# Optimization experiments

Hardware: AMD Instinct MI355X
Metric: run time of the kernel (lower is better)

Reference implementation:

```python
import jax, jax.numpy as jnp
import numpy as np

B, T, D, H = 8, 2048, 1024, 1024

def setup_inputs() -> dict:
    key = jax.random.key(0)
    k1, k2, k3, k4 = jax.random.split(key, 4)
    scale = 1.0 / np.sqrt(D)
    return {
        "x": jax.random.normal(k1, (B, T, D), dtype=jnp.float32),
        "Wq": jax.random.normal(k2, (D, H), dtype=jnp.float32) * scale,
        "Wk": jax.random.normal(k3, (D, H), dtype=jnp.float32) * scale,
        "Wv": jax.random.normal(k4, (D, H), dtype=jnp.float32) * scale,
    }

def reference(x, Wq, Wk, Wv):
    # Single-head causal self-attention (dropout in eval mode = identity)
    q = jnp.einsum('btd,dh->bth', x, Wq)
    k = jnp.einsum('btd,dh->bth', x, Wk)
    v = jnp.einsum('btd,dh->bth', x, Wv)
    inv_sqrt_h = 1.0 / jnp.sqrt(jnp.asarray(q.shape[-1], q.dtype))
    scores = jnp.einsum('bqh,bkh->bqk', q, k) * inv_sqrt_h  # [B, T, T]
    Tq = scores.shape[-1]
    causal = jnp.tril(jnp.ones((Tq, Tq), dtype=bool))
    scores = jnp.where(causal, scores, jnp.asarray(-jnp.inf, scores.dtype))
    weights = jax.nn.softmax(scores, axis=-1)
    return jnp.einsum('bqk,bkh->bqh', weights, v)
```

## Files before the change

kernel.cpp:

```cpp
#include <hip/hip_runtime.h>

#define Bn 8
#define Tn 2048
#define Dn 1024
#define Hn 1024
#define Mn (Bn * Tn)

typedef __attribute__((ext_vector_type(8))) short bf16x8;
typedef __attribute__((ext_vector_type(4))) short short4v;
typedef __attribute__((ext_vector_type(16))) float f32x16;

__device__ __forceinline__ unsigned short f2bf(float f) {
  union { float f; unsigned int u; } v; v.f = f;
  unsigned int u = v.u;
  u += 0x7FFFu + ((u >> 16) & 1u);
  return (unsigned short)(u >> 16);
}
__device__ __forceinline__ float bf2f(unsigned short h) {
  union { unsigned int u; float f; } v; v.u = ((unsigned int)h) << 16;
  return v.f;
}

__device__ __forceinline__ void gload_lds16(const unsigned short* g, unsigned short* l) {
  __builtin_amdgcn_global_load_lds((const __attribute__((address_space(1))) void*)g,
                                   (__attribute__((address_space(3))) void*)l, 16, 0, 0);
}

__device__ __forceinline__ void stage128x32s(const unsigned short* gbase, size_t row_stride,
                                             unsigned short* lds, int wave, int lane) {
#pragma unroll
  for (int c = 0; c < 2; ++c) {
    int rl = c * 16 + (lane >> 2);
    int pos = (lane & 3) ^ (rl & 3);
    const unsigned short* g = gbase + (size_t)(wave * 32 + rl) * row_stride + pos * 8;
    gload_lds16(g, lds + (wave * 32 + c * 16) * 32);
  }
}
__device__ __forceinline__ void stage128x64s(const unsigned short* gbase, size_t row_stride,
                                             unsigned short* lds0, unsigned short* lds1,
                                             int wave, int lane) {
  stage128x32s(gbase, row_stride, lds0, wave, lane);
  stage128x32s(gbase + 32, row_stride, lds1, wave, lane);
}

__device__ __forceinline__ void mma_bk32(const unsigned short* lA, const unsigned short* lB,
                                         int wr, int wc, int l32, int half,
                                         f32x16 acc[2][2]) {
#pragma unroll
  for (int kk = 0; kk < 2; ++kk) {
    const int pos = (kk * 2 + half) ^ (l32 & 3);
    bf16x8 af[2], bfr[2];
#pragma unroll
    for (int m = 0; m < 2; ++m)
      af[m] = *(const bf16x8*)&lA[(wr + m * 32 + l32) * 32 + pos * 8];
#pragma unroll
    for (int n = 0; n < 2; ++n)
      bfr[n] = *(const bf16x8*)&lB[(wc + n * 32 + l32) * 32 + pos * 8];
#pragma unroll
    for (int m = 0; m < 2; ++m)
#pragma unroll
      for (int n = 0; n < 2; ++n)
        acc[m][n] = __builtin_amdgcn_mfma_f32_32x32x16_bf16(af[m], bfr[n], acc[m][n], 0, 0, 0);
  }
}

__global__ __launch_bounds__(256) void k_convert(const float* __restrict__ in,
                                                 unsigned short* __restrict__ out, int n4) {
  int idx = blockIdx.x * 256 + threadIdx.x;
  if (idx >= n4) return;
  float4 v = ((const float4*)in)[idx];
  short4v o;
  o.x = (short)f2bf(v.x); o.y = (short)f2bf(v.y);
  o.z = (short)f2bf(v.z); o.w = (short)f2bf(v.w);
  *(short4v*)(out + (size_t)idx * 4) = o;
}

__global__ __launch_bounds__(256) void k_cvt_w_t(const float* __restrict__ W0,
                                                 const float* __restrict__ W1,
                                                 const float* __restrict__ W2,
                                                 unsigned short* __restrict__ Wt3) {
  const int n0 = blockIdx.x * 64, k0 = blockIdx.y * 64, w = blockIdx.z;
  const float* W = (w == 0) ? W0 : (w == 1) ? W1 : W2;
  unsigned short* Wt = Wt3 + (size_t)w * Hn * Dn;
  __shared__ unsigned short lT[64 * 65];
  const int tid = threadIdx.x;
#pragma unroll
  for (int p = 0; p < 2; ++p) {
    int o = tid + p * 256;
    int r = o >> 3, c = (o & 7) * 8;
    const float* src = W + (size_t)(k0 + r) * Hn + n0 + c;
    float4 v0 = *(const float4*)src;
    float4 v1 = *(const float4*)(src + 4);
    unsigned short* d = &lT[r * 65 + c];
    d[0] = f2bf(v0.x); d[1] = f2bf(v0.y); d[2] = f2bf(v0.z); d[3] = f2bf(v0.w);
    d[4] = f2bf(v1.x); d[5] = f2bf(v1.y); d[6] = f2bf(v1.z); d[7] = f2bf(v1.w);
  }
  __syncthreads();
#pragma unroll
  for (int p = 0; p < 2; ++p) {
    int o = tid + p * 256;
    int r2 = o >> 3, c2 = (o & 7) * 8;
    bf16x8 v;
#pragma unroll
    for (int s = 0; s < 8; ++s) v[s] = (short)lT[(c2 + s) * 65 + r2];
    *(bf16x8*)(Wt + (size_t)(n0 + r2) * Dn + k0 + c2) = v;
  }
}

__global__ __launch_bounds__(256) void gemm_qkv(const unsigned short* __restrict__ A,
                                                const unsigned short* __restrict__ Wt3,
                                                unsigned short* __restrict__ Q,
                                                unsigned short* __restrict__ Kb,
                                                unsigned short* __restrict__ Vt) {
  const int f = blockIdx.x;
  const int c = f & 7;
  const int q = f >> 3;
  const int nn = q % 24;
  const int w = nn >> 3;
  const int n0 = (nn & 7) * 128;
  const int m0 = ((q / 24) * 8 + c) * 128;
  const unsigned short* B = Wt3 + (size_t)w * Hn * Dn;
  __shared__ unsigned short lA[2][128 * 32];
  __shared__ unsigned short lB[2][128 * 32];
  const int tid = threadIdx.x;
  const int lane = tid & 63, wave = tid >> 6;
  const int wr = (wave >> 1) * 64, wc = (wave & 1) * 64;
  const int l32 = lane & 31, half = lane >> 5;

  f32x16 acc[2][2];
#pragma unroll
  for (int m = 0; m < 2; ++m)
#pragma unroll
    for (int n = 0; n < 2; ++n) acc[m][n] = (f32x16)(0.f);

  for (int kt = 0; kt < Dn / 64; ++kt) {
    stage128x64s(A + (size_t)m0 * Dn + kt * 64, Dn, lA[0], lA[1], wave, lane);
    stage128x64s(B + (size_t)n0 * Dn + kt * 64, Dn, lB[0], lB[1], wave, lane);
    __syncthreads();
    mma_bk32(lA[0], lB[0], wr, wc, l32, half, acc);
    mma_bk32(lA[1], lB[1], wr, wc, l32, half, acc);
    __syncthreads();
  }
  if (w != 2) {
    unsigned short* C = (w == 0) ? Q : Kb;
#pragma unroll
    for (int m = 0; m < 2; ++m)
#pragma unroll
      for (int n = 0; n < 2; ++n) {
        int col = n0 + wc + n * 32 + l32;
#pragma unroll
        for (int qd = 0; qd < 4; ++qd) {
          int rb = m0 + wr + m * 32 + 8 * qd + 4 * half;
#pragma unroll
          for (int rr = 0; rr < 4; ++rr)
            C[(size_t)(rb + rr) * Hn + col] = f2bf(acc[m][n][qd * 4 + rr]);
        }
      }
  } else {
    const int bb = m0 >> 11;
    const int tb = m0 & 2047;
#pragma unroll
    for (int m = 0; m < 2; ++m)
#pragma unroll
      for (int n = 0; n < 2; ++n) {
        int h = n0 + wc + n * 32 + l32;
#pragma unroll
        for (int qd = 0; qd < 4; ++qd) {
          int t0 = tb + wr + m * 32 + 8 * qd + 4 * half;
          short4v o;
          o.x = (short)f2bf(acc[m][n][qd * 4 + 0]);
          o.y = (short)f2bf(acc[m][n][qd * 4 + 1]);
          o.z = (short)f2bf(acc[m][n][qd * 4 + 2]);
          o.w = (short)f2bf(acc[m][n][qd * 4 + 3]);
          *(short4v*)(Vt + ((size_t)bb * Hn + h) * Tn + t0) = o;
        }
      }
  }
}

__global__ __launch_bounds__(256) void gemm_scores(const unsigned short* __restrict__ Q,
                                                   const unsigned short* __restrict__ K,
                                                   unsigned short* __restrict__ S) {
  const int f = blockIdx.x;
  const int b = f & 7;
  const int q = f >> 3;
  const int rt = 15 - (q & 15);
  const int ct = q >> 4;
  if (ct > rt) return;
  const int j0 = ct * 128, i0 = rt * 128;
  const unsigned short* Qb = Q + (size_t)b * Tn * Hn;
  const unsigned short* Kp = K + (size_t)b * Tn * Hn;
  unsigned short* Sb = S + (size_t)b * Tn * Tn;
  __shared__ unsigned short lA[2][128 * 32];
  __shared__ unsigned short lB[2][128 * 32];
  const int tid = threadIdx.x;
  const int lane = tid & 63, wave = tid >> 6;
  const int wr = (wave >> 1) * 64, wc = (wave & 1) * 64;
  const int l32 = lane & 31, half = lane >> 5;

  f32x16 acc[2][2];
#pragma unroll
  for (int m = 0; m < 2; ++m)
#pragma unroll
    for (int n = 0; n < 2; ++n) acc[m][n] = (f32x16)(0.f);

  for (int kt = 0; kt < Hn / 64; ++kt) {
    stage128x64s(Qb + (size_t)i0 * Hn + kt * 64, Hn, lA[0], lA[1], wave, lane);
    stage128x64s(Kp + (size_t)j0 * Hn + kt * 64, Hn, lB[0], lB[1], wave, lane);
    __syncthreads();
    mma_bk32(lA[0], lB[0], wr, wc, l32, half, acc);
    mma_bk32(lA[1], lB[1], wr, wc, l32, half, acc);
    __syncthreads();
  }
#pragma unroll
  for (int m = 0; m < 2; ++m)
#pragma unroll
    for (int n = 0; n < 2; ++n) {
      int col = j0 + wc + n * 32 + l32;
#pragma unroll
      for (int qd = 0; qd < 4; ++qd) {
        int rb = i0 + wr + m * 32 + 8 * qd + 4 * half;
#pragma unroll
        for (int rr = 0; rr < 4; ++rr) {
          int row = rb + rr;
          float e = (col <= row) ? __expf(acc[m][n][qd * 4 + rr] * 0.03125f) : 0.f;
          Sb[(size_t)row * Tn + col] = f2bf(e);
        }
      }
    }
}

__global__ __launch_bounds__(256) void k_rowsum(const unsigned short* __restrict__ S,
                                                float* __restrict__ l) {
  const int b = blockIdx.y;
  const int i = blockIdx.x * 4 + (threadIdx.x >> 6);
  const int lane = threadIdx.x & 63;
  const unsigned short* row = S + ((size_t)b * Tn + i) * (size_t)Tn;
  const int npad = ((i >> 7) + 1) << 7;
  float s = 0.f;
  for (int j0 = 0; j0 < npad; j0 += 512) {
    int j = j0 + lane * 8;
    if (j < npad) {
      bf16x8 v = *(const bf16x8*)(row + j);
#pragma unroll
      for (int t = 0; t < 8; ++t) s += bf2f((unsigned short)v[t]);
    }
  }
#pragma unroll
  for (int off = 32; off > 0; off >>= 1) s += __shfl_down(s, off);
  if (lane == 0) l[(size_t)b * Tn + i] = s;
}

__global__ __launch_bounds__(256) void gemm_out(const unsigned short* __restrict__ P,
                                                const unsigned short* __restrict__ Vt,
                                                const float* __restrict__ lbuf,
                                                float* __restrict__ O) {
  const int f = blockIdx.x;
  const int b = f & 7;
  const int q = f >> 3;
  const int n0 = (q & 7) * 128;
  const int rt = 15 - (q >> 3);
  const int i0 = rt * 128;
  const int nkt = (rt + 1) * 2;
  const unsigned short* Pb = P + (size_t)b * Tn * Tn;
  const unsigned short* Vb = Vt + (size_t)b * Tn * Hn;
  __shared__ unsigned short lA[2][128 * 32];
  __shared__ unsigned short lB[2][128 * 32];
  const int tid = threadIdx.x;
  const int lane = tid & 63, wave = tid >> 6;
  const int wr = (wave >> 1) * 64, wc = (wave & 1) * 64;
  const int l32 = lane & 31, half = lane >> 5;

  f32x16 acc[2][2];
#pragma unroll
  for (int m = 0; m < 2; ++m)
#pragma unroll
    for (int n = 0; n < 2; ++n) acc[m][n] = (f32x16)(0.f);

  for (int kt = 0; kt < nkt; ++kt) {
    stage128x64s(Pb + (size_t)i0 * Tn + kt * 64, Tn, lA[0], lA[1], wave, lane);
    stage128x64s(Vb + (size_t)n0 * Tn + kt * 64, Tn, lB[0], lB[1], wave, lane);
    __syncthreads();
    mma_bk32(lA[0], lB[0], wr, wc, l32, half, acc);
    mma_bk32(lA[1], lB[1], wr, wc, l32, half, acc);
    __syncthreads();
  }
#pragma unroll
  for (int m = 0; m < 2; ++m)
#pragma unroll
    for (int n = 0; n < 2; ++n) {
      int col = n0 + wc + n * 32 + l32;
#pragma unroll
      for (int qd = 0; qd < 4; ++qd) {
        int rb = i0 + wr + m * 32 + 8 * qd + 4 * half;
        float4 lv = *(const float4*)&lbuf[(size_t)b * Tn + rb];
#pragma unroll
        for (int rr = 0; rr < 4; ++rr) {
          float inv = 1.f / ((&lv.x)[rr]);
          O[((size_t)b * Tn + rb + rr) * Hn + col] = acc[m][n][qd * 4 + rr] * inv;
        }
      }
    }
}

extern "C" void kernel_launch(void* const* d_in, const int* in_sizes, int n_in,
                              void* d_out, int out_size, void* d_ws, size_t ws_size,
                              hipStream_t stream) {
  const float* x  = (const float*)d_in[0];
  const float* Wq = (const float*)d_in[1];
  const float* Wk = (const float*)d_in[2];
  const float* Wv = (const float*)d_in[3];
  float* out = (float*)d_out;

  char* ws = (char*)d_ws;
  const size_t MiB = 1024 * 1024;
  unsigned short* Wt3 = (unsigned short*)(ws + 0 * MiB);
  unsigned short* xb  = (unsigned short*)(ws + 6 * MiB);
  unsigned short* Qb  = (unsigned short*)(ws + 38 * MiB);
  unsigned short* Kb  = (unsigned short*)(ws + 70 * MiB);
  unsigned short* Vt  = (unsigned short*)(ws + 102 * MiB);
  unsigned short* S   = (unsigned short*)(ws + 134 * MiB);
  float*          lrow = (float*)(ws + 6 * MiB);

  {
    int n4 = (Mn * Dn) / 4;
    k_convert<<<dim3(n4 / 256), 256, 0, stream>>>(x, xb, n4);
  }
  {
    dim3 g(Hn / 64, Dn / 64, 3);
    k_cvt_w_t<<<g, 256, 0, stream>>>(Wq, Wk, Wv, Wt3);
  }
  {
    gemm_qkv<<<dim3(3072), 256, 0, stream>>>(xb, Wt3, Qb, Kb, Vt);
  }
  {
    gemm_scores<<<dim3(2048), 256, 0, stream>>>(Qb, Kb, S);
  }
  {
    k_rowsum<<<dim3(Tn / 4, Bn), 256, 0, stream>>>(S, lrow);
  }
  {
    gemm_out<<<dim3(1024), 256, 0, stream>>>(S, Vt, lrow, out);
  }
}
```

Baseline: 373.3 us.

## Retile QKV GEMM to 256x256 blocks with double-buffered LDS pipeline

The QKV projection GEMM moves from 128x128 tiles with 256 threads to 256x256 tiles with 512 threads, 16x16x32 MFMAs and a 128x64 per-wave sub-tile. A double-buffered global-to-LDS pipeline overlaps the next K-slice load with compute, using explicit vmcnt waits and s_setprio around MFMA bursts. The LDS swizzle gains an extra XOR term to reduce bank conflicts; this swizzle is shared with the other GEMMs. The aim is more data reuse per tile and hidden load latency, at the cost of higher register and LDS pressure and fewer blocks.

New measurement: 349.2 us. -6.4%, faster.

```diff
diff --git a/kernel.cpp b/kernel.cpp
--- a/kernel.cpp
+++ b/kernel.cpp
@@ -9,6 +9,7 @@
 typedef __attribute__((ext_vector_type(8))) short bf16x8;
 typedef __attribute__((ext_vector_type(4))) short short4v;
 typedef __attribute__((ext_vector_type(16))) float f32x16;
+typedef __attribute__((ext_vector_type(4))) float f32x4;
 
 __device__ __forceinline__ unsigned short f2bf(float f) {
   union { float f; unsigned int u; } v; v.f = f;
@@ -26,12 +27,13 @@
                                    (__attribute__((address_space(3))) void*)l, 16, 0, 0);
 }
 
+
 __device__ __forceinline__ void stage128x32s(const unsigned short* gbase, size_t row_stride,
                                              unsigned short* lds, int wave, int lane) {
 #pragma unroll
   for (int c = 0; c < 2; ++c) {
     int rl = c * 16 + (lane >> 2);
-    int pos = (lane & 3) ^ (rl & 3);
+    int pos = (lane & 3) ^ (rl & 3) ^ ((rl >> 2) & 3);
     const unsigned short* g = gbase + (size_t)(wave * 32 + rl) * row_stride + pos * 8;
     gload_lds16(g, lds + (wave * 32 + c * 16) * 32);
   }
@@ -43,12 +45,23 @@
   stage128x32s(gbase + 32, row_stride, lds1, wave, lane);
 }
 
+__device__ __forceinline__ void stage256x32s(const unsigned short* gbase, size_t row_stride,
+                                             unsigned short* lds, int wave, int lane) {
+#pragma unroll
+  for (int c = 0; c < 2; ++c) {
+    int rl = c * 16 + (lane >> 2);
+    int pos = (lane & 3) ^ (rl & 3) ^ ((rl >> 2) & 3);
+    const unsigned short* g = gbase + (size_t)(wave * 32 + rl) * row_stride + pos * 8;
+    gload_lds16(g, lds + (wave * 32 + c * 16) * 32);
+  }
+}
+
 __device__ __forceinline__ void mma_bk32(const unsigned short* lA, const unsigned short* lB,
                                          int wr, int wc, int l32, int half,
                                          f32x16 acc[2][2]) {
 #pragma unroll
   for (int kk = 0; kk < 2; ++kk) {
-    const int pos = (kk * 2 + half) ^ (l32 & 3);
+    const int pos = (kk * 2 + half) ^ (l32 & 3) ^ ((l32 >> 2) & 3);
     bf16x8 af[2], bfr[2];
 #pragma unroll
     for (int m = 0; m < 2; ++m)
@@ -107,74 +120,149 @@
   }
 }
 
-__global__ __launch_bounds__(256) void gemm_qkv(const unsigned short* __restrict__ A,
-                                                const unsigned short* __restrict__ Wt3,
-                                                unsigned short* __restrict__ Q,
-                                                unsigned short* __restrict__ Kb,
-                                                unsigned short* __restrict__ Vt) {
+__global__ __launch_bounds__(512, 2) void gemm_qkv(const unsigned short* __restrict__ A,
+                                                   const unsigned short* __restrict__ Wt3,
+                                                   unsigned short* __restrict__ Q,
+                                                   unsigned short* __restrict__ Kb,
+                                                   unsigned short* __restrict__ Vt) {
   const int f = blockIdx.x;
   const int c = f & 7;
   const int q = f >> 3;
-  const int nn = q % 24;
-  const int w = nn >> 3;
-  const int n0 = (nn & 7) * 128;
-  const int m0 = ((q / 24) * 8 + c) * 128;
-  const unsigned short* B = Wt3 + (size_t)w * Hn * Dn;
-  __shared__ unsigned short lA[2][128 * 32];
-  __shared__ unsigned short lB[2][128 * 32];
+  const int nn = q % 12;
+  const int w = nn >> 2;
+  const int n0 = (nn & 3) * 256;
+  const int m0 = ((q / 12) * 8 + c) * 256;
+  const unsigned short* Bw = Wt3 + (size_t)w * Hn * Dn;
+  __shared__ unsigned short lds[2][4][256 * 32];
   const int tid = threadIdx.x;
   const int lane = tid & 63, wave = tid >> 6;
-  const int wr = (wave >> 1) * 64, wc = (wave & 1) * 64;
-  const int l32 = lane & 31, half = lane >> 5;
-
-  f32x16 acc[2][2];
-#pragma unroll
-  for (int m = 0; m < 2; ++m)
-#pragma unroll
-    for (int n = 0; n < 2; ++n) acc[m][n] = (f32x16)(0.f);
-
-  for (int kt = 0; kt < Dn / 64; ++kt) {
-    stage128x64s(A + (size_t)m0 * Dn + kt * 64, Dn, lA[0], lA[1], wave, lane);
-    stage128x64s(B + (size_t)n0 * Dn + kt * 64, Dn, lB[0], lB[1], wave, lane);
-    __syncthreads();
-    mma_bk32(lA[0], lB[0], wr, wc, l32, half, acc);
-    mma_bk32(lA[1], lB[1], wr, wc, l32, half, acc);
-    __syncthreads();
-  }
+  const int wr = (wave >> 2) * 128;
+  const int wc = (wave & 3) * 64;
+  const int rl15 = lane & 15, l4 = lane >> 4;
+  const int csw = (l4 ^ (lane & 3) ^ ((lane >> 2) & 3)) & 3;
+
+  f32x4 acc[8][4];
+#pragma unroll
+  for (int m = 0; m < 8; ++m)
+#pragma unroll
+    for (int n = 0; n < 4; ++n) acc[m][n] = (f32x4)(0.f);
+
+  const unsigned short* Ab = A + (size_t)m0 * Dn;
+  const unsigned short* Bb = Bw + (size_t)n0 * Dn;
+
+  auto stage_tile = [&](int kt, int d) {
+#pragma unroll
+    for (int h = 0; h < 2; ++h) {
+      stage256x32s(Ab + kt * 64 + h * 32, Dn, &lds[d][h][0], wave, lane);
+      stage256x32s(Bb + kt * 64 + h * 32, Dn, &lds[d][2 + h][0], wave, lane);
+    }
+  };
+
+  auto compute_tile = [&](int d) {
+    const unsigned short* pa = &lds[d][0][0];
+    const unsigned short* pb = &lds[d][2][0];
+    bf16x8 af[4][2], bf[4][2];
+#pragma unroll
+    for (int m = 0; m < 4; ++m)
+#pragma unroll
+      for (int h = 0; h < 2; ++h)
+        af[m][h] = *(const bf16x8*)&pa[h * 8192 + (wr + m * 16 + rl15) * 32 + csw * 8];
+#pragma unroll
+    for (int n = 0; n < 2; ++n)
+#pragma unroll
+      for (int h = 0; h < 2; ++h)
+        bf[n][h] = *(const bf16x8*)&pb[h * 8192 + (wc + n * 16 + rl15) * 32 + csw * 8];
+    __builtin_amdgcn_s_setprio(1);
+#pragma unroll
+    for (int m = 0; m < 4; ++m)
+#pragma unroll
+      for (int n = 0; n < 2; ++n)
+#pragma unroll
+        for (int h = 0; h < 2; ++h)
+          acc[m][n] = __builtin_amdgcn_mfma_f32_16x16x32_bf16(af[m][h], bf[n][h], acc[m][n], 0, 0, 0);
+    __builtin_amdgcn_s_setprio(0);
+#pragma unroll
+    for (int n = 2; n < 4; ++n)
+#pragma unroll
+      for (int h = 0; h < 2; ++h)
+        bf[n][h] = *(const bf16x8*)&pb[h * 8192 + (wc + n * 16 + rl15) * 32 + csw * 8];
+    __builtin_amdgcn_s_setprio(1);
+#pragma unroll
+    for (int m = 0; m < 4; ++m)
+#pragma unroll
+      for (int n = 2; n < 4; ++n)
+#pragma unroll
+        for (int h = 0; h < 2; ++h)
+          acc[m][n] = __builtin_amdgcn_mfma_f32_16x16x32_bf16(af[m][h], bf[n][h], acc[m][n], 0, 0, 0);
+    __builtin_amdgcn_s_setprio(0);
+#pragma unroll
+    for (int m = 0; m < 4; ++m)
+#pragma unroll
+      for (int h = 0; h < 2; ++h)
+        af[m][h] = *(const bf16x8*)&pa[h * 8192 + (wr + (m + 4) * 16 + rl15) * 32 + csw * 8];
+    __builtin_amdgcn_s_setprio(1);
+#pragma unroll
+    for (int m = 0; m < 4; ++m)
+#pragma unroll
+      for (int n = 2; n < 4; ++n)
+#pragma unroll
+        for (int h = 0; h < 2; ++h)
+          acc[m + 4][n] = __builtin_amdgcn_mfma_f32_16x16x32_bf16(af[m][h], bf[n][h], acc[m + 4][n], 0, 0, 0);
+    __builtin_amdgcn_s_setprio(0);
+    __builtin_amdgcn_s_setprio(1);
+#pragma unroll
+    for (int m = 0; m < 4; ++m)
+#pragma unroll
+      for (int n = 0; n < 2; ++n)
+#pragma unroll
+        for (int h = 0; h < 2; ++h)
+          acc[m + 4][n] = __builtin_amdgcn_mfma_f32_16x16x32_bf16(af[m][h], bf[n][h], acc[m + 4][n], 0, 0, 0);
+    __builtin_amdgcn_s_setprio(0);
+  };
+
+  stage_tile(0, 0);
+  for (int kt = 0; kt < Dn / 64 - 1; ++kt) {
+    const int d = kt & 1;
+    __builtin_amdgcn_s_barrier();
+    stage_tile(kt + 1, d ^ 1);
+    asm volatile("s_waitcnt vmcnt(8)" ::: "memory");
+    __builtin_amdgcn_s_barrier();
+    compute_tile(d);
+  }
+  asm volatile("s_waitcnt vmcnt(0)" ::: "memory");
+  __builtin_amdgcn_s_barrier();
+  compute_tile(1);
+
   if (w != 2) {
-    unsigned short* C = (w == 0) ? Q : Kb;
-#pragma unroll
-    for (int m = 0; m < 2; ++m)
-#pragma unroll
-      for (int n = 0; n < 2; ++n) {
-        int col = n0 + wc + n * 32 + l32;
-#pragma unroll
-        for (int qd = 0; qd < 4; ++qd) {
-          int rb = m0 + wr + m * 32 + 8 * qd + 4 * half;
-#pragma unroll
-          for (int rr = 0; rr < 4; ++rr)
-            C[(size_t)(rb + rr) * Hn + col] = f2bf(acc[m][n][qd * 4 + rr]);
-        }
+    unsigned short* Cp = (w == 0) ? Q : Kb;
+#pragma unroll
+    for (int m = 0; m < 8; ++m) {
+      const int row = m0 + wr + m * 16 + l4 * 4;
+#pragma unroll
+      for (int n = 0; n < 4; ++n) {
+        const int col = n0 + wc + n * 16 + rl15;
+#pragma unroll
+        for (int r = 0; r < 4; ++r)
+          Cp[(size_t)(row + r) * Hn + col] = f2bf(acc[m][n][r]);
       }
+    }
   } else {
     const int bb = m0 >> 11;
     const int tb = m0 & 2047;
 #pragma unroll
-    for (int m = 0; m < 2; ++m)
-#pragma unroll
-      for (int n = 0; n < 2; ++n) {
-        int h = n0 + wc + n * 32 + l32;
-#pragma unroll
-        for (int qd = 0; qd < 4; ++qd) {
-          int t0 = tb + wr + m * 32 + 8 * qd + 4 * half;
-          short4v o;
-          o.x = (short)f2bf(acc[m][n][qd * 4 + 0]);
-          o.y = (short)f2bf(acc[m][n][qd * 4 + 1]);
-          o.z = (short)f2bf(acc[m][n][qd * 4 + 2]);
-          o.w = (short)f2bf(acc[m][n][qd * 4 + 3]);
-          *(short4v*)(Vt + ((size_t)bb * Hn + h) * Tn + t0) = o;
-        }
+    for (int m = 0; m < 8; ++m) {
+      const int t0 = tb + wr + m * 16 + l4 * 4;
+#pragma unroll
+      for (int n = 0; n < 4; ++n) {
+        const int h = n0 + wc + n * 16 + rl15;
+        short4v o;
+        o.x = (short)f2bf(acc[m][n][0]);
+        o.y = (short)f2bf(acc[m][n][1]);
+        o.z = (short)f2bf(acc[m][n][2]);
+        o.w = (short)f2bf(acc[m][n][3]);
+        *(short4v*)(Vt + ((size_t)bb * Hn + h) * Tn + t0) = o;
       }
+    }
   }
 }
 
@@ -331,7 +419,7 @@
     k_cvt_w_t<<<g, 256, 0, stream>>>(Wq, Wk, Wv, Wt3);
   }
   {
-    gemm_qkv<<<dim3(3072), 256, 0, stream>>>(xb, Wt3, Qb, Kb, Vt);
+    gemm_qkv<<<dim3(768), 512, 0, stream>>>(xb, Wt3, Qb, Kb, Vt);
   }
   {
     gemm_scores<<<dim3(2048), 256, 0, stream>>>(Qb, Kb, S);
```

## Use single-wave 128x128 tiles with async double-buffered LDS and fused rowsum

Applied to the files above, without the earlier changes.

All three GEMMs now run on one 64-thread wave per 128x128 tile. Each wave holds an 8x8 grid of 16x16x32 MFMA accumulators and double-buffers LDS using global_load_lds, with vmcnt waits in place of __syncthreads. The scores kernel launches only the causal lower-triangle tiles, indexed with a triangular mapping, and folds the row-sum into its epilogue via atomics, which removes the separate rowsum kernel. In exchange each block has far fewer threads, uses very high register pressure from 256 accumulator floats, and gives up occupancy and latency hiding.

New measurement: 453.2 us. +21.4%, slower.

```diff
diff --git a/kernel.cpp b/kernel.cpp
--- a/kernel.cpp
+++ b/kernel.cpp
@@ -8,7 +8,7 @@
 
 typedef __attribute__((ext_vector_type(8))) short bf16x8;
 typedef __attribute__((ext_vector_type(4))) short short4v;
-typedef __attribute__((ext_vector_type(16))) float f32x16;
+typedef __attribute__((ext_vector_type(4))) float f32x4;
 
 __device__ __forceinline__ unsigned short f2bf(float f) {
   union { float f; unsigned int u; } v; v.f = f;
@@ -26,43 +26,50 @@
                                    (__attribute__((address_space(3))) void*)l, 16, 0, 0);
 }
 
-__device__ __forceinline__ void stage128x32s(const unsigned short* gbase, size_t row_stride,
-                                             unsigned short* lds, int wave, int lane) {
-#pragma unroll
-  for (int c = 0; c < 2; ++c) {
+
+__device__ __forceinline__ void stg128(const unsigned short* g, size_t stride,
+                                       unsigned short* lds, int lane) {
+#pragma unroll
+  for (int c = 0; c < 8; ++c) {
     int rl = c * 16 + (lane >> 2);
-    int pos = (lane & 3) ^ (rl & 3);
-    const unsigned short* g = gbase + (size_t)(wave * 32 + rl) * row_stride + pos * 8;
-    gload_lds16(g, lds + (wave * 32 + c * 16) * 32);
-  }
-}
-__device__ __forceinline__ void stage128x64s(const unsigned short* gbase, size_t row_stride,
-                                             unsigned short* lds0, unsigned short* lds1,
-                                             int wave, int lane) {
-  stage128x32s(gbase, row_stride, lds0, wave, lane);
-  stage128x32s(gbase + 32, row_stride, lds1, wave, lane);
-}
-
-__device__ __forceinline__ void mma_bk32(const unsigned short* lA, const unsigned short* lB,
-                                         int wr, int wc, int l32, int half,
-                                         f32x16 acc[2][2]) {
-#pragma unroll
-  for (int kk = 0; kk < 2; ++kk) {
-    const int pos = (kk * 2 + half) ^ (l32 & 3);
-    bf16x8 af[2], bfr[2];
-#pragma unroll
-    for (int m = 0; m < 2; ++m)
-      af[m] = *(const bf16x8*)&lA[(wr + m * 32 + l32) * 32 + pos * 8];
-#pragma unroll
-    for (int n = 0; n < 2; ++n)
-      bfr[n] = *(const bf16x8*)&lB[(wc + n * 32 + l32) * 32 + pos * 8];
-#pragma unroll
-    for (int m = 0; m < 2; ++m)
-#pragma unroll
-      for (int n = 0; n < 2; ++n)
-        acc[m][n] = __builtin_amdgcn_mfma_f32_32x32x16_bf16(af[m], bfr[n], acc[m][n], 0, 0, 0);
-  }
-}
+    int pos = (lane & 3) ^ (rl & 3) ^ ((rl >> 2) & 3);
+    gload_lds16(g + (size_t)rl * stride + pos * 8, lds + c * 16 * 32);
+  }
+}
+
+__device__ __forceinline__ void rd8(const unsigned short* p, int rl15, int csw, bf16x8 fr[8]) {
+#pragma unroll
+  for (int m = 0; m < 8; ++m)
+    fr[m] = *(const bf16x8*)&p[(m * 16 + rl15) * 32 + csw * 8];
+}
+
+#define W_VM16 asm volatile("s_waitcnt vmcnt(16)" ::: "memory")
+#define W_VM0  asm volatile("s_waitcnt vmcnt(0)" ::: "memory")
+#define W_LGKM0 asm volatile("s_waitcnt lgkmcnt(0)" ::: "memory")
+
+#define KLOOP(Ag, sA, Bg, sB, nt, lds, lane, rl15, csw, acc)                              \
+  {                                                                                        \
+    stg128((Ag), (sA), &(lds)[0][0][0], lane);                                             \
+    stg128((Bg), (sB), &(lds)[0][1][0], lane);                                             \
+    _Pragma("unroll 1")                                                                    \
+    for (int t = 0; t < (nt); ++t) {                                                       \
+      W_LGKM0;                                                                             \
+      const int ts = (t + 1 < (nt)) ? t + 1 : (nt)-1;                                      \
+      stg128((Ag) + (size_t)ts * 32, (sA), &(lds)[(t + 1) & 1][0][0], lane);               \
+      stg128((Bg) + (size_t)ts * 32, (sB), &(lds)[(t + 1) & 1][1][0], lane);               \
+      W_VM16;                                                                              \
+      bf16x8 a[8], b[8];                                                                   \
+      rd8(&(lds)[t & 1][0][0], rl15, csw, a);                                              \
+      rd8(&(lds)[t & 1][1][0], rl15, csw, b);                                              \
+      _Pragma("unroll")                                                                    \
+      for (int m = 0; m < 8; ++m)                                                          \
+        _Pragma("unroll")                                                                  \
+        for (int n = 0; n < 8; ++n)                                                        \
+          acc[m][n] = __builtin_amdgcn_mfma_f32_16x16x32_bf16(a[m], b[n], acc[m][n], 0, 0, 0); \
+    }                                                                                      \
+    W_VM0;                                                                                 \
+    W_LGKM0;                                                                               \
+  }
 
 __global__ __launch_bounds__(256) void k_convert(const float* __restrict__ in,
                                                  unsigned short* __restrict__ out, int n4) {
@@ -107,11 +114,11 @@
   }
 }
 
-__global__ __launch_bounds__(256) void gemm_qkv(const unsigned short* __restrict__ A,
-                                                const unsigned short* __restrict__ Wt3,
-                                                unsigned short* __restrict__ Q,
-                                                unsigned short* __restrict__ Kb,
-                                                unsigned short* __restrict__ Vt) {
+__global__ __launch_bounds__(64, 1) void gemm_qkv(const unsigned short* __restrict__ A,
+                                                  const unsigned short* __restrict__ Wt3,
+                                                  unsigned short* __restrict__ Q,
+                                                  unsigned short* __restrict__ Kb,
+                                                  unsigned short* __restrict__ Vt) {
   const int f = blockIdx.x;
   const int c = f & 7;
   const int q = f >> 3;
@@ -119,188 +126,148 @@
   const int w = nn >> 3;
   const int n0 = (nn & 7) * 128;
   const int m0 = ((q / 24) * 8 + c) * 128;
-  const unsigned short* B = Wt3 + (size_t)w * Hn * Dn;
-  __shared__ unsigned short lA[2][128 * 32];
-  __shared__ unsigned short lB[2][128 * 32];
-  const int tid = threadIdx.x;
-  const int lane = tid & 63, wave = tid >> 6;
-  const int wr = (wave >> 1) * 64, wc = (wave & 1) * 64;
-  const int l32 = lane & 31, half = lane >> 5;
-
-  f32x16 acc[2][2];
-#pragma unroll
-  for (int m = 0; m < 2; ++m)
-#pragma unroll
-    for (int n = 0; n < 2; ++n) acc[m][n] = (f32x16)(0.f);
-
-  for (int kt = 0; kt < Dn / 64; ++kt) {
-    stage128x64s(A + (size_t)m0 * Dn + kt * 64, Dn, lA[0], lA[1], wave, lane);
-    stage128x64s(B + (size_t)n0 * Dn + kt * 64, Dn, lB[0], lB[1], wave, lane);
-    __syncthreads();
-    mma_bk32(lA[0], lB[0], wr, wc, l32, half, acc);
-    mma_bk32(lA[1], lB[1], wr, wc, l32, half, acc);
-    __syncthreads();
-  }
+  const unsigned short* Ag = A + (size_t)m0 * Dn;
+  const unsigned short* Bg = Wt3 + (size_t)w * Hn * Dn + (size_t)n0 * Dn;
+  __shared__ unsigned short lds[2][2][128 * 32];
+  const int lane = threadIdx.x & 63;
+  const int rl15 = lane & 15, l4 = lane >> 4;
+  const int csw = (l4 ^ (lane & 3) ^ ((lane >> 2) & 3)) & 3;
+
+  f32x4 acc[8][8];
+#pragma unroll
+  for (int m = 0; m < 8; ++m)
+#pragma unroll
+    for (int n = 0; n < 8; ++n) acc[m][n] = (f32x4)(0.f);
+
+  KLOOP(Ag, Dn, Bg, Dn, Dn / 32, lds, lane, rl15, csw, acc);
+
   if (w != 2) {
-    unsigned short* C = (w == 0) ? Q : Kb;
-#pragma unroll
-    for (int m = 0; m < 2; ++m)
-#pragma unroll
-      for (int n = 0; n < 2; ++n) {
-        int col = n0 + wc + n * 32 + l32;
-#pragma unroll
-        for (int qd = 0; qd < 4; ++qd) {
-          int rb = m0 + wr + m * 32 + 8 * qd + 4 * half;
-#pragma unroll
-          for (int rr = 0; rr < 4; ++rr)
-            C[(size_t)(rb + rr) * Hn + col] = f2bf(acc[m][n][qd * 4 + rr]);
-        }
+    unsigned short* Cp = (w == 0) ? Q : Kb;
+#pragma unroll
+    for (int m = 0; m < 8; ++m) {
+      const int row = m0 + m * 16 + l4 * 4;
+#pragma unroll
+      for (int n = 0; n < 8; ++n) {
+        const int col = n0 + n * 16 + rl15;
+#pragma unroll
+        for (int r = 0; r < 4; ++r)
+          Cp[(size_t)(row + r) * Hn + col] = f2bf(acc[m][n][r]);
       }
+    }
   } else {
     const int bb = m0 >> 11;
     const int tb = m0 & 2047;
 #pragma unroll
-    for (int m = 0; m < 2; ++m)
-#pragma unroll
-      for (int n = 0; n < 2; ++n) {
-        int h = n0 + wc + n * 32 + l32;
-#pragma unroll
-        for (int qd = 0; qd < 4; ++qd) {
-          int t0 = tb + wr + m * 32 + 8 * qd + 4 * half;
-          short4v o;
-          o.x = (short)f2bf(acc[m][n][qd * 4 + 0]);
-          o.y = (short)f2bf(acc[m][n][qd * 4 + 1]);
-          o.z = (short)f2bf(acc[m][n][qd * 4 + 2]);
-          o.w = (short)f2bf(acc[m][n][qd * 4 + 3]);
-          *(short4v*)(Vt + ((size_t)bb * Hn + h) * Tn + t0) = o;
-        }
+    for (int m = 0; m < 8; ++m) {
+      const int t0 = tb + m * 16 + l4 * 4;
+#pragma unroll
+      for (int n = 0; n < 8; ++n) {
+        const int h = n0 + n * 16 + rl15;
+        short4v o;
+        o.x = (short)f2bf(acc[m][n][0]);
+        o.y = (short)f2bf(acc[m][n][1]);
+        o.z = (short)f2bf(acc[m][n][2]);
+        o.w = (short)f2bf(acc[m][n][3]);
+        *(short4v*)(Vt + ((size_t)bb * Hn + h) * Tn + t0) = o;
       }
-  }
-}
-
-__global__ __launch_bounds__(256) void gemm_scores(const unsigned short* __restrict__ Q,
-                                                   const unsigned short* __restrict__ K,
-                                                   unsigned short* __restrict__ S) {
+    }
+  }
+}
+
+__global__ __launch_bounds__(64, 1) void gemm_scores(const unsigned short* __restrict__ Q,
+                                                     const unsigned short* __restrict__ K,
+                                                     unsigned short* __restrict__ S,
+                                                     float* __restrict__ lrow) {
   const int f = blockIdx.x;
   const int b = f & 7;
-  const int q = f >> 3;
-  const int rt = 15 - (q & 15);
-  const int ct = q >> 4;
-  if (ct > rt) return;
-  const int j0 = ct * 128, i0 = rt * 128;
-  const unsigned short* Qb = Q + (size_t)b * Tn * Hn;
-  const unsigned short* Kp = K + (size_t)b * Tn * Hn;
+  const int u = f >> 3;
+  int rt = (int)((sqrtf(8.f * (float)u + 1.f) - 1.f) * 0.5f);
+  if ((rt + 1) * (rt + 2) / 2 <= u) ++rt;
+  if (rt * (rt + 1) / 2 > u) --rt;
+  const int ct = u - rt * (rt + 1) / 2;
+  const int i0 = rt * 128, j0 = ct * 128;
+  const unsigned short* Ag = Q + (size_t)b * Tn * Hn + (size_t)i0 * Hn;
+  const unsigned short* Bg = K + (size_t)b * Tn * Hn + (size_t)j0 * Hn;
   unsigned short* Sb = S + (size_t)b * Tn * Tn;
-  __shared__ unsigned short lA[2][128 * 32];
-  __shared__ unsigned short lB[2][128 * 32];
-  const int tid = threadIdx.x;
-  const int lane = tid & 63, wave = tid >> 6;
-  const int wr = (wave >> 1) * 64, wc = (wave & 1) * 64;
-  const int l32 = lane & 31, half = lane >> 5;
-
-  f32x16 acc[2][2];
-#pragma unroll
-  for (int m = 0; m < 2; ++m)
-#pragma unroll
-    for (int n = 0; n < 2; ++n) acc[m][n] = (f32x16)(0.f);
-
-  for (int kt = 0; kt < Hn / 64; ++kt) {
-    stage128x64s(Qb + (size_t)i0 * Hn + kt * 64, Hn, lA[0], lA[1], wave, lane);
-    stage128x64s(Kp + (size_t)j0 * Hn + kt * 64, Hn, lB[0], lB[1], wave, lane);
-    __syncthreads();
-    mma_bk32(lA[0], lB[0], wr, wc, l32, half, acc);
-    mma_bk32(lA[1], lB[1], wr, wc, l32, half, acc);
-    __syncthreads();
-  }
-#pragma unroll
-  for (int m = 0; m < 2; ++m)
-#pragma unroll
-    for (int n = 0; n < 2; ++n) {
-      int col = j0 + wc + n * 32 + l32;
-#pragma unroll
-      for (int qd = 0; qd < 4; ++qd) {
-        int rb = i0 + wr + m * 32 + 8 * qd + 4 * half;
-#pragma unroll
-        for (int rr = 0; rr < 4; ++rr) {
-          int row = rb + rr;
-          float e = (col <= row) ? __expf(acc[m][n][qd * 4 + rr] * 0.03125f) : 0.f;
-          Sb[(size_t)row * Tn + col] = f2bf(e);
-        }
+  __shared__ unsigned short lds[2][2][128 * 32];
+  const int lane = threadIdx.x & 63;
+  const int rl15 = lane & 15, l4 = lane >> 4;
+  const int csw = (l4 ^ (lane & 3) ^ ((lane >> 2) & 3)) & 3;
+
+  f32x4 acc[8][8];
+#pragma unroll
+  for (int m = 0; m < 8; ++m)
+#pragma unroll
+    for (int n = 0; n < 8; ++n) acc[m][n] = (f32x4)(0.f);
+
+  KLOOP(Ag, Hn, Bg, Hn, Hn / 32, lds, lane, rl15, csw, acc);
+
+#pragma unroll
+  for (int m = 0; m < 8; ++m) {
+    const int row = i0 + m * 16 + l4 * 4;
+    float rs[4] = {0.f, 0.f, 0.f, 0.f};
+#pragma unroll
+    for (int n = 0; n < 8; ++n) {
+      const int col = j0 + n * 16 + rl15;
+#pragma unroll
+      for (int r = 0; r < 4; ++r) {
+        float e = (col <= row + r) ? __expf(acc[m][n][r] * 0.03125f) : 0.f;
+        unsigned short eb = f2bf(e);
+        Sb[(size_t)(row + r) * Tn + col] = eb;
+        rs[r] += bf2f(eb);
       }
     }
-}
-
-__global__ __launch_bounds__(256) void k_rowsum(const unsigned short* __restrict__ S,
-                                                float* __restrict__ l) {
-  const int b = blockIdx.y;
-  const int i = blockIdx.x * 4 + (threadIdx.x >> 6);
-  const int lane = threadIdx.x & 63;
-  const unsigned short* row = S + ((size_t)b * Tn + i) * (size_t)Tn;
-  const int npad = ((i >> 7) + 1) << 7;
-  float s = 0.f;
-  for (int j0 = 0; j0 < npad; j0 += 512) {
-    int j = j0 + lane * 8;
-    if (j < npad) {
-      bf16x8 v = *(const bf16x8*)(row + j);
-#pragma unroll
-      for (int t = 0; t < 8; ++t) s += bf2f((unsigned short)v[t]);
-    }
-  }
-#pragma unroll
-  for (int off = 32; off > 0; off >>= 1) s += __shfl_down(s, off);
-  if (lane == 0) l[(size_t)b * Tn + i] = s;
-}
-
-__global__ __launch_bounds__(256) void gemm_out(const unsigned short* __restrict__ P,
-                                                const unsigned short* __restrict__ Vt,
-                                                const float* __restrict__ lbuf,
-                                                float* __restrict__ O) {
+#pragma unroll
+    for (int r = 0; r < 4; ++r) {
+#pragma unroll
+      for (int msk = 1; msk < 16; msk <<= 1)
+        rs[r] += __shfl_xor(rs[r], msk);
+      if (rl15 == 0)
+        atomicAdd(&lrow[(size_t)b * Tn + row + r], rs[r]);
+    }
+  }
+}
+
+__global__ __launch_bounds__(64, 1) void gemm_out(const unsigned short* __restrict__ P,
+                                                  const unsigned short* __restrict__ Vt,
+                                                  const float* __restrict__ lbuf,
+                                                  float* __restrict__ O) {
   const int f = blockIdx.x;
   const int b = f & 7;
   const int q = f >> 3;
   const int n0 = (q & 7) * 128;
   const int rt = 15 - (q >> 3);
   const int i0 = rt * 128;
-  const int nkt = (rt + 1) * 2;
-  const unsigned short* Pb = P + (size_t)b * Tn * Tn;
-  const unsigned short* Vb = Vt + (size_t)b * Tn * Hn;
-  __shared__ unsigned short lA[2][128 * 32];
-  __shared__ unsigned short lB[2][128 * 32];
-  const int tid = threadIdx.x;
-  const int lane = tid & 63, wave = tid >> 6;
-  const int wr = (wave >> 1) * 64, wc = (wave & 1) * 64;
-  const int l32 = lane & 31, half = lane >> 5;
-
-  f32x16 acc[2][2];
-#pragma unroll
-  for (int m = 0; m < 2; ++m)
-#pragma unroll
-    for (int n = 0; n < 2; ++n) acc[m][n] = (f32x16)(0.f);
-
-  for (int kt = 0; kt < nkt; ++kt) {
-    stage128x64s(Pb + (size_t)i0 * Tn + kt * 64, Tn, lA[0], lA[1], wave, lane);
-    stage128x64s(Vb + (size_t)n0 * Tn + kt * 64, Tn, lB[0], lB[1], wave, lane);
-    __syncthreads();
-    mma_bk32(lA[0], lB[0], wr, wc, l32, half, acc);
-    mma_bk32(lA[1], lB[1], wr, wc, l32, half, acc);
-    __syncthreads();
-  }
-#pragma unroll
-  for (int m = 0; m < 2; ++m)
-#pragma unroll
-    for (int n = 0; n < 2; ++n) {
-      int col = n0 + wc + n * 32 + l32;
-#pragma unroll
-      for (int qd = 0; qd < 4; ++qd) {
-        int rb = i0 + wr + m * 32 + 8 * qd + 4 * half;
-        float4 lv = *(const float4*)&lbuf[(size_t)b * Tn + rb];
-#pragma unroll
-        for (int rr = 0; rr < 4; ++rr) {
-          float inv = 1.f / ((&lv.x)[rr]);
-          O[((size_t)b * Tn + rb + rr) * Hn + col] = acc[m][n][qd * 4 + rr] * inv;
-        }
-      }
-    }
+  const int nkt = (rt + 1) * 4;
+  const unsigned short* Ag = P + (size_t)b * Tn * Tn + (size_t)i0 * Tn;
+  const unsigned short* Bg = Vt + (size_t)b * Tn * Hn + (size_t)n0 * Tn;
+  __shared__ unsigned short lds[2][2][128 * 32];
+  const int lane = threadIdx.x & 63;
+  const int rl15 = lane & 15, l4 = lane >> 4;
+  const int csw = (l4 ^ (lane & 3) ^ ((lane >> 2) & 3)) & 3;
+
+  f32x4 acc[8][8];
+#pragma unroll
+  for (int m = 0; m < 8; ++m)
+#pragma unroll
+    for (int n = 0; n < 8; ++n) acc[m][n] = (f32x4)(0.f);
+
+  KLOOP(Ag, Tn, Bg, Tn, nkt, lds, lane, rl15, csw, acc);
+
+#pragma unroll
+  for (int m = 0; m < 8; ++m) {
+    const int rb = i0 + m * 16 + l4 * 4;
+    float4 lv = *(const float4*)&lbuf[(size_t)b * Tn + rb];
+    const float inv0 = 1.f / lv.x, inv1 = 1.f / lv.y, inv2 = 1.f / lv.z, inv3 = 1.f / lv.w;
+#pragma unroll
+    for (int n = 0; n < 8; ++n) {
+      const int col = n0 + n * 16 + rl15;
+      O[((size_t)b * Tn + rb + 0) * Hn + col] = acc[m][n][0] * inv0;
+      O[((size_t)b * Tn + rb + 1) * Hn + col] = acc[m][n][1] * inv1;
+      O[((size_t)b * Tn + rb + 2) * Hn + col] = acc[m][n][2] * inv2;
+      O[((size_t)b * Tn + rb + 3) * Hn + col] = acc[m][n][3] * inv3;
+    }
+  }
 }
 
 extern "C" void kernel_launch(void* const* d_in, const int* in_sizes, int n_in,
@@ -331,15 +298,13 @@
     k_cvt_w_t<<<g, 256, 0, stream>>>(Wq, Wk, Wv, Wt3);
   }
   {
-    gemm_qkv<<<dim3(3072), 256, 0, stream>>>(xb, Wt3, Qb, Kb, Vt);
-  }
-  {
-    gemm_scores<<<dim3(2048), 256, 0, stream>>>(Qb, Kb, S);
-  }
-  {
-    k_rowsum<<<dim3(Tn / 4, Bn), 256, 0, stream>>>(S, lrow);
-  }
-  {
-    gemm_out<<<dim3(1024), 256, 0, stream>>>(S, Vt, lrow, out);
-  }
-}
+    gemm_qkv<<<dim3(3072), 64, 0, stream>>>(xb, Wt3, Qb, Kb, Vt);
+  }
+  hipMemsetAsync(lrow, 0, (size_t)Bn * Tn * sizeof(float), stream);
+  {
+    gemm_scores<<<dim3(1088), 64, 0, stream>>>(Qb, Kb, S, lrow);
+  }
+  {
+    gemm_out<<<dim3(1024), 64, 0, stream>>>(S, Vt, lrow, out);
+  }
+}
```
